# Performance work log

Hardware: AMD Instinct MI355X
Metric: run time of the kernel (lower is better)

Reference implementation:

```python
import jax, jax.numpy as jnp
import numpy as np
from jax import lax

LAMBD = 1.0
KAPPA = 0.1
N_ITERS = 400  # fixed unroll count; PGD converges well within this for these scales


def _project_simplex(v):
    # Euclidean projection of each row of v onto {w : w >= 0, sum(w) = 1}.
    n = v.shape[-1]
    u = -jnp.sort(-v, axis=-1)                       # descending sort
    css = jnp.cumsum(u, axis=-1)
    j = jnp.arange(1, n + 1, dtype=v.dtype)
    cond = u + (1.0 - css) / j > 0                   # monotone condition; rho = #True
    rho = jnp.sum(cond, axis=-1, keepdims=True)      # [B,1], always >= 1
    css_rho = jnp.take_along_axis(css, rho - 1, axis=-1)
    tau = (css_rho - 1.0) / rho.astype(v.dtype)
    return jnp.maximum(v - tau, 0.0)


def _solve_robust_mvo(mu, U, A):
    # min_w -mu'w + kappa*||A w||_2 + (lambd/2)*||U w||_2^2  s.t. w in simplex
    B, n = mu.shape
    G1 = jnp.einsum('bij,bik->bjk', U, U)            # U^T U, [B,n,n]
    G2 = jnp.einsum('bij,bik->bjk', A, A)            # A^T A, [B,n,n]
    # Lipschitz upper bound via Frobenius norms -> safe fixed step size
    froU2 = jnp.sum(U * U, axis=(-2, -1), keepdims=False)[:, None]   # ||U||_F^2, [B,1]
    froA = jnp.sqrt(jnp.sum(A * A, axis=(-2, -1)))[:, None]          # ||A||_F,   [B,1]
    step = 1.0 / (LAMBD * froU2 + KAPPA * froA + 1.0)

    w0 = jnp.full((B, n), 1.0 / n, dtype=mu.dtype)

    def body(w, _):
        g1w = jnp.einsum('bij,bj->bi', G1, w)        # U^T U w
        g2w = jnp.einsum('bij,bj->bi', G2, w)        # A^T A w
        nrm = jnp.sqrt(jnp.maximum(jnp.sum(w * g2w, axis=-1, keepdims=True), 1e-12))
        grad = -mu + LAMBD * g1w + KAPPA * g2w / nrm
        w_new = _project_simplex(w - step * grad)
        return w_new, None

    w, _ = lax.scan(body, w0, None, length=N_ITERS)
    # mirror the torch post-processing: clamp + renormalize
    w = jnp.maximum(w, 0.0)
    return w / (jnp.sum(w, axis=-1, keepdims=True) + 1e-12)


def setup_inputs() -> dict:
    key = jax.random.key(0)
    k1, k2, k3 = jax.random.split(key, 3)
    B, n = 512, 256
    mu = jax.random.normal(k1, (B, n), dtype=jnp.float32)
    U = jax.random.normal(k2, (B, n, n), dtype=jnp.float32)
    A = jax.random.normal(k3, (B, n, n), dtype=jnp.float32)
    return {"mu": mu, "U": U, "A": A}


def reference(mu, U, A):
    return _solve_robust_mvo(mu, U, A)
```

## Files before the change

kernel.cpp:

```cpp
#include <hip/hip_runtime.h>
#include <math.h>

#define NB 512
#define NN 256
#define N_ITERS 400
#define KAPPA_F 0.1f

typedef _Float16 half2_t __attribute__((ext_vector_type(2)));
typedef _Float16 half8_t __attribute__((ext_vector_type(8)));

__device__ inline float fdot2f(half2_t a, half2_t b, float c) {
#if __has_builtin(__builtin_amdgcn_fdot2)
  return __builtin_amdgcn_fdot2(a, b, c, false);
#else
  return (float)a.x * (float)b.x + (float)a.y * (float)b.y + c;
#endif
}


#define PAIR(V, K) __builtin_shufflevector(V, V, 2*(K), 2*(K)+1)

template <int CTRL>
__device__ inline float dpp_addt(float v) {
  int s = __builtin_amdgcn_update_dpp(0, __float_as_int(v), CTRL, 0xF, 0xF, true);
  return v + __int_as_float(s);
}
__device__ inline float wave_sum(float v) {
  v = dpp_addt<0xB1>(v);
  v = dpp_addt<0x4E>(v);
  v = dpp_addt<0x141>(v);
  v = dpp_addt<0x140>(v);
  v += __shfl_xor(v, 16, 64);
  v += __shfl_xor(v, 32, 64);
  return v;
}
__device__ inline void wave_sum2(float& a, float& b) {
  a = dpp_addt<0xB1>(a);  b = dpp_addt<0xB1>(b);
  a = dpp_addt<0x4E>(a);  b = dpp_addt<0x4E>(b);
  a = dpp_addt<0x141>(a); b = dpp_addt<0x141>(b);
  a = dpp_addt<0x140>(a); b = dpp_addt<0x140>(b);
  a += __shfl_xor(a, 16, 64); b += __shfl_xor(b, 16, 64);
  a += __shfl_xor(a, 32, 64); b += __shfl_xor(b, 32, 64);
}

#define DECLROW(P) half2_t P##0,P##1,P##2,P##3,P##4,P##5,P##6,P##7, \
                           P##8,P##9,P##10,P##11,P##12,P##13,P##14,P##15;

#define ZA(J) cA##J.x=0.f; cA##J.y=0.f; cA##J.z=0.f; cA##J.w=0.f;
#define ZB(J) cB##J.x=0.f; cB##J.y=0.f; cB##J.z=0.f; cB##J.w=0.f;
#define ZALL() ZA(0) ZA(1) ZA(2) ZA(3) ZA(4) ZA(5) ZA(6) ZA(7) \
               ZB(0) ZB(1) ZB(2) ZB(3) ZB(4) ZB(5) ZB(6) ZB(7)
#define GMA(J,F) { cA##J.x=fmaf(a0,F.x,cA##J.x); cA##J.y=fmaf(a0,F.y,cA##J.y); \
                   cA##J.z=fmaf(a0,F.z,cA##J.z); cA##J.w=fmaf(a0,F.w,cA##J.w); }
#define GMB(J,F) { cB##J.x=fmaf(a1,F.x,cB##J.x); cB##J.y=fmaf(a1,F.y,cB##J.y); \
                   cB##J.z=fmaf(a1,F.z,cB##J.z); cB##J.w=fmaf(a1,F.w,cB##J.w); }

#define GRAM2(SRC, RB, DOFRO) do { \
  const float4* __restrict__ src4 = (const float4*)(SRC); \
  ZALL() \
  float4 st0 = src4[t], st1 = src4[512 + t]; \
  _Pragma("unroll 1") \
  for (int kt = 0; kt < 16; ++kt) { \
    __syncthreads(); \
    ((float4*)As)[t] = st0; \
    ((float4*)As)[512 + t] = st1; \
    if (DOFRO) { fro += st0.x*st0.x + st0.y*st0.y + st0.z*st0.z + st0.w*st0.w; \
                 fro += st1.x*st1.x + st1.y*st1.y + st1.z*st1.z + st1.w*st1.w; } \
    __syncthreads(); \
    if (kt < 15) { st0 = src4[(kt+1)*1024 + t]; st1 = src4[(kt+1)*1024 + 512 + t]; } \
    _Pragma("unroll 1") \
    for (int k = 0; k < 16; ++k) { \
      const float* rowp = As + k * NN; \
      float a0 = rowp[(RB) + lane]; \
      float a1 = rowp[(RB) + 64 + lane]; \
      const float4* rp4 = (const float4*)(rowp + 32 * wv); \
      { float4 f0=rp4[0], f1=rp4[1], f2=rp4[2], f3=rp4[3]; \
        GMA(0,f0) GMA(1,f1) GMA(2,f2) GMA(3,f3) \
        GMB(0,f0) GMB(1,f1) GMB(2,f2) GMB(3,f3) } \
      { float4 f4=rp4[4], f5=rp4[5], f6=rp4[6], f7=rp4[7]; \
        GMA(4,f4) GMA(5,f5) GMA(6,f6) GMA(7,f7) \
        GMB(4,f4) GMB(5,f5) GMB(6,f6) GMB(7,f7) } \
    } \
  } \
} while (0)

#define GRAM1(SRC, RB, DOFRO) do { \
  const float4* __restrict__ src4 = (const float4*)(SRC); \
  ZA(0) ZA(1) ZA(2) ZA(3) ZA(4) ZA(5) ZA(6) ZA(7) \
  float4 st = src4[t]; \
  _Pragma("unroll 1") \
  for (int kt = 0; kt < 32; ++kt) { \
    __syncthreads(); \
    ((float4*)As)[t] = st; \
    if (DOFRO) fro += st.x*st.x + st.y*st.y + st.z*st.z + st.w*st.w; \
    __syncthreads(); \
    if (kt < 31) st = src4[(kt + 1) * 512 + t]; \
    _Pragma("unroll 1") \
    for (int k = 0; k < 8; ++k) { \
      const float* rowp = As + k * NN; \
      float a0 = rowp[(RB) + lane]; \
      const float4* rp4 = (const float4*)(rowp + 32 * wv); \
      { float4 f0=rp4[0], f1=rp4[1], f2=rp4[2], f3=rp4[3]; \
        GMA(0,f0) GMA(1,f1) GMA(2,f2) GMA(3,f3) } \
      { float4 f4=rp4[4], f5=rp4[5], f6=rp4[6], f7=rp4[7]; \
        GMA(4,f4) GMA(5,f5) GMA(6,f6) GMA(7,f7) } \
    } \
  } \
} while (0)

#define PACK4(PA, PB, C, J4, DIAG) { \
  float x0=C.x, x1=C.y, x2=C.z, x3=C.w; \
  const int cb = 32*wv + 4*(J4); \
  if (cb+0==row_) { DIAG[row_]=x0; x0=0.f; } \
  if (cb+1==row_) { DIAG[row_]=x1; x1=0.f; } \
  if (cb+2==row_) { DIAG[row_]=x2; x2=0.f; } \
  if (cb+3==row_) { DIAG[row_]=x3; x3=0.f; } \
  PA.x=(_Float16)x0; PA.y=(_Float16)x1; \
  PB.x=(_Float16)x2; PB.y=(_Float16)x3; }

#define PACKROW(P, CP, DIAG) { \
  PACK4(P##0,  P##1,  c##CP##0, 0, DIAG) \
  PACK4(P##2,  P##3,  c##CP##1, 1, DIAG) \
  PACK4(P##4,  P##5,  c##CP##2, 2, DIAG) \
  PACK4(P##6,  P##7,  c##CP##3, 3, DIAG) \
  PACK4(P##8,  P##9,  c##CP##4, 4, DIAG) \
  PACK4(P##10, P##11, c##CP##5, 5, DIAG) \
  PACK4(P##12, P##13, c##CP##6, 6, DIAG) \
  PACK4(P##14, P##15, c##CP##7, 7, DIAG) }

#define DOTROW(ACC, P) \
  ACC = fdot2f(P##0,  PAIR(uh0,0), ACC); \
  ACC = fdot2f(P##1,  PAIR(uh0,1), ACC); \
  ACC = fdot2f(P##2,  PAIR(uh0,2), ACC); \
  ACC = fdot2f(P##3,  PAIR(uh0,3), ACC); \
  ACC = fdot2f(P##4,  PAIR(uh1,0), ACC); \
  ACC = fdot2f(P##5,  PAIR(uh1,1), ACC); \
  ACC = fdot2f(P##6,  PAIR(uh1,2), ACC); \
  ACC = fdot2f(P##7,  PAIR(uh1,3), ACC); \
  ACC = fdot2f(P##8,  PAIR(uh2,0), ACC); \
  ACC = fdot2f(P##9,  PAIR(uh2,1), ACC); \
  ACC = fdot2f(P##10, PAIR(uh2,2), ACC); \
  ACC = fdot2f(P##11, PAIR(uh2,3), ACC); \
  ACC = fdot2f(P##12, PAIR(uh3,0), ACC); \
  ACC = fdot2f(P##13, PAIR(uh3,1), ACC); \
  ACC = fdot2f(P##14, PAIR(uh3,2), ACC); \
  ACC = fdot2f(P##15, PAIR(uh3,3), ACC);

#define COMB(I) { \
  const int rr = 64 * (I) + lane; \
  float2 x0 = parts[rr],          x1 = parts[NN + rr]; \
  float2 x2 = parts[2*NN + rr],   x3 = parts[3*NN + rr]; \
  float2 x4 = parts[4*NN + rr],   x5 = parts[5*NN + rr]; \
  float2 x6 = parts[6*NN + rr],   x7 = parts[7*NN + rr]; \
  q1##I = ((x0.x+x1.x)+(x2.x+x3.x))+((x4.x+x5.x)+(x6.x+x7.x)); \
  q2##I = ((x0.y+x1.y)+(x2.y+x3.y))+((x4.y+x5.y)+(x6.y+x7.y)); }

__global__
__attribute__((amdgpu_flat_work_group_size(512, 512)))
__attribute__((amdgpu_waves_per_eu(1, 2)))
void mvo_kernel(const float* __restrict__ mu,
                const float* __restrict__ U,
                const float* __restrict__ A,
                float* __restrict__ out)
{
  __shared__ alignas(16) float2 parts[8 * NN];
  __shared__ alignas(16) float    wsf[NN];
  __shared__ alignas(16) _Float16 whs[NN];
  __shared__ float mus[NN];
  __shared__ float diag1[NN];
  __shared__ float diag2[NN];
  __shared__ float dslot[8];
  __shared__ float slotA[8];
  __shared__ float slotB[8];
  __shared__ float taus;
  __shared__ int   doneflag;

  float* As = (float*)parts;

  const int t    = threadIdx.x;
  const int b    = blockIdx.x;
  const int lane = t & 63;
  const int wv   = t >> 6;

  const float* __restrict__ Ub = U + (size_t)b * NN * NN;
  const float* __restrict__ Ab = A + (size_t)b * NN * NN;

  if (t == 0) { doneflag = 0; taus = -1e30f; }
  if (t < NN) mus[t] = mu[b * NN + t];

  DECLROW(e0_) DECLROW(e1_) DECLROW(e2_) DECLROW(e3_)
  DECLROW(h0_) DECLROW(h1_) DECLROW(h2_) DECLROW(h3_)
  float4 cA0,cA1,cA2,cA3,cA4,cA5,cA6,cA7;
  float4 cB0,cB1,cB2,cB3,cB4,cB5,cB6,cB7;
  float fro, d1, d2;

  fro = 0.f;
  GRAM2(Ab, 0, 1);
  { const int row_ = lane;        PACKROW(h0_, A, diag2) }
  { const int row_ = 64 + lane;   PACKROW(h1_, B, diag2) }
  GRAM2(Ab, 128, 0);
  { const int row_ = 128 + lane;  PACKROW(h2_, A, diag2) }
  { const int row_ = 192 + lane;  PACKROW(h3_, B, diag2) }
  d2 = fro;
  fro = 0.f;
  GRAM1(Ub, 0, 1);
  { const int row_ = lane;        PACKROW(e0_, A, diag1) }
  GRAM1(Ub, 64, 0);
  { const int row_ = 64 + lane;   PACKROW(e1_, A, diag1) }
  GRAM1(Ub, 128, 0);
  { const int row_ = 128 + lane;  PACKROW(e2_, A, diag1) }
  GRAM1(Ub, 192, 0);
  { const int row_ = 192 + lane;  PACKROW(e3_, A, diag1) }
  d1 = fro;

  #pragma unroll
  for (int m = 1; m < 64; m <<= 1) {
    d1 += __shfl_xor(d1, m, 64);
    d2 += __shfl_xor(d2, m, 64);
  }
  if (lane == 0) { slotA[wv] = d1; slotB[wv] = d2; }
  if (t < NN) { wsf[t] = 1.0f / 256.0f; whs[t] = (_Float16)(1.0f / 256.0f); }
  __syncthreads();
  float froU2 = 0.f, froA2 = 0.f;
  #pragma unroll
  for (int k = 0; k < 8; ++k) { froU2 += slotA[k]; froA2 += slotB[k]; }
  const float step = 1.0f / (froU2 + KAPPA_F * sqrtf(froA2) + 1.0f);

  const half8_t* whp = (const half8_t*)whs + 4 * wv;
  const int dsel = lane >> 5;

  #pragma unroll 1
  for (int it = 0; it < N_ITERS; ++it) {
    half8_t uh0 = whp[0], uh1 = whp[1], uh2 = whp[2], uh3 = whp[3];
    float p10=0.f, p11=0.f, p12=0.f, p13=0.f;
    float p20=0.f, p21=0.f, p22=0.f, p23=0.f;
    DOTROW(p10, e0_) DOTROW(p11, e1_) DOTROW(p12, e2_) DOTROW(p13, e3_)
    DOTROW(p20, h0_) DOTROW(p21, h1_) DOTROW(p22, h2_) DOTROW(p23, h3_)

    float w_r0 = wsf[lane],       w_r1 = wsf[64 + lane];
    float w_r2 = wsf[128 + lane], w_r3 = wsf[192 + lane];
    if (wv == dsel)     { p10 = fmaf(diag1[lane],     w_r0, p10);
                          p20 = fmaf(diag2[lane],     w_r0, p20); }
    if (wv == 2 + dsel) { p11 = fmaf(diag1[64+lane],  w_r1, p11);
                          p21 = fmaf(diag2[64+lane],  w_r1, p21); }
    if (wv == 4 + dsel) { p12 = fmaf(diag1[128+lane], w_r2, p12);
                          p22 = fmaf(diag2[128+lane], w_r2, p22); }
    if (wv == 6 + dsel) { p13 = fmaf(diag1[192+lane], w_r3, p13);
                          p23 = fmaf(diag2[192+lane], w_r3, p23); }
    float dpart = fmaf(p20, w_r0, fmaf(p21, w_r1, fmaf(p22, w_r2, p23 * w_r3)));
    dpart = wave_sum(dpart);
    parts[wv * NN + lane]       = make_float2(p10, p20);
    parts[wv * NN + 64 + lane]  = make_float2(p11, p21);
    parts[wv * NN + 128 + lane] = make_float2(p12, p22);
    parts[wv * NN + 192 + lane] = make_float2(p13, p23);
    if (lane == 0) dslot[wv] = dpart;
    __syncthreads();

    if (wv == 0) {
      float q10, q11, q12, q13, q20, q21, q22, q23;
      COMB(0) COMB(1) COMB(2) COMB(3)
      float dot = ((dslot[0]+dslot[1])+(dslot[2]+dslot[3]))
                + ((dslot[4]+dslot[5])+(dslot[6]+dslot[7]));
      float nrm = sqrtf(fmaxf(dot, 1e-12f));
      float kon = KAPPA_F / nrm;
      float v0 = w_r0 - step * (q10 + kon * q20 - mus[lane]);
      float v1 = w_r1 - step * (q11 + kon * q21 - mus[64 + lane]);
      float v2 = w_r2 - step * (q12 + kon * q22 - mus[128 + lane]);
      float v3 = w_r3 - step * (q13 + kon * q23 - mus[192 + lane]);
      float tau = taus;
      float cprev = -1.f;
      #pragma unroll 1
      for (int ms = 0; ms < 24; ++ms) {
        float s2 = (v0 > tau ? v0 : 0.f) + (v1 > tau ? v1 : 0.f)
                 + (v2 > tau ? v2 : 0.f) + (v3 > tau ? v3 : 0.f);
        float c2 = (v0 > tau ? 1.f : 0.f) + (v1 > tau ? 1.f : 0.f)
                 + (v2 > tau ? 1.f : 0.f) + (v3 > tau ? 1.f : 0.f);
        wave_sum2(s2, c2);
        if (c2 == cprev) break;
        tau = (s2 - 1.0f) / c2;
        cprev = c2;
      }
      float nw0 = fmaxf(v0 - tau, 0.f);
      float nw1 = fmaxf(v1 - tau, 0.f);
      float nw2 = fmaxf(v2 - tau, 0.f);
      float nw3 = fmaxf(v3 - tau, 0.f);
      int same = (nw0 == w_r0) && (nw1 == w_r1) && (nw2 == w_r2) && (nw3 == w_r3);
      int conv = __all(same);
      wsf[lane]       = nw0; wsf[64 + lane]  = nw1;
      wsf[128 + lane] = nw2; wsf[192 + lane] = nw3;
      whs[lane]       = (_Float16)nw0; whs[64 + lane]  = (_Float16)nw1;
      whs[128 + lane] = (_Float16)nw2; whs[192 + lane] = (_Float16)nw3;
      if (lane == 0) { taus = tau; doneflag = conv; }
    }
    __syncthreads();
    if (doneflag) break;
  }

  if (wv == 0) {
    float w_0 = wsf[lane],       w_1 = wsf[64 + lane];
    float w_2 = wsf[128 + lane], w_3 = wsf[192 + lane];
    float s = wave_sum(w_0 + w_1 + w_2 + w_3);
    float inv = 1.0f / (s + 1e-12f);
    float* ob = out + b * NN;
    ob[lane]        = w_0 * inv;
    ob[64 + lane]   = w_1 * inv;
    ob[128 + lane]  = w_2 * inv;
    ob[192 + lane]  = w_3 * inv;
  }
}

extern "C" void kernel_launch(void* const* d_in, const int* in_sizes, int n_in,
                              void* d_out, int out_size, void* d_ws, size_t ws_size,
                              hipStream_t stream) {
  const float* mu = (const float*)d_in[0];
  const float* U  = (const float*)d_in[1];
  const float* A  = (const float*)d_in[2];
  float* out = (float*)d_out;
  hipLaunchKernelGGL(mvo_kernel, dim3(NB), dim3(512), 0, stream, mu, U, A, out);
}
```

Measured before the change: 2.133 ms.

## Replicate projection step in every wave to drop second barrier per iteration

Instead of wave 0 alone combining partial sums and projecting onto the simplex while the other waves wait, every wave now does the redundant combine, norm and projection itself. Each wave keeps w in registers and writes its fp16 copy to a private LDS slot. The partial-sum buffer is double-buffered, so only one __syncthreads per iteration remains. The wave reduction now uses row_bcast DPP plus a readlane instead of shuffles, giving a uniform scalar result. This trades eight-fold redundant projection work and extra LDS reads for fewer barriers and less idle time.

```diff
diff --git a/kernel.cpp b/kernel.cpp
--- a/kernel.cpp
+++ b/kernel.cpp
@@ -20,27 +20,19 @@
 
 #define PAIR(V, K) __builtin_shufflevector(V, V, 2*(K), 2*(K)+1)
 
-template <int CTRL>
-__device__ inline float dpp_addt(float v) {
-  int s = __builtin_amdgcn_update_dpp(0, __float_as_int(v), CTRL, 0xF, 0xF, true);
+template <int CTRL, int RMASK>
+__device__ inline float dpp_add(float v) {
+  int s = __builtin_amdgcn_update_dpp(0, __float_as_int(v), CTRL, RMASK, 0xF, true);
   return v + __int_as_float(s);
 }
-__device__ inline float wave_sum(float v) {
-  v = dpp_addt<0xB1>(v);
-  v = dpp_addt<0x4E>(v);
-  v = dpp_addt<0x141>(v);
-  v = dpp_addt<0x140>(v);
-  v += __shfl_xor(v, 16, 64);
-  v += __shfl_xor(v, 32, 64);
-  return v;
-}
-__device__ inline void wave_sum2(float& a, float& b) {
-  a = dpp_addt<0xB1>(a);  b = dpp_addt<0xB1>(b);
-  a = dpp_addt<0x4E>(a);  b = dpp_addt<0x4E>(b);
-  a = dpp_addt<0x141>(a); b = dpp_addt<0x141>(b);
-  a = dpp_addt<0x140>(a); b = dpp_addt<0x140>(b);
-  a += __shfl_xor(a, 16, 64); b += __shfl_xor(b, 16, 64);
-  a += __shfl_xor(a, 32, 64); b += __shfl_xor(b, 32, 64);
+__device__ inline float wave_sum_sgpr(float v) {
+  v = dpp_add<0xB1, 0xF>(v);
+  v = dpp_add<0x4E, 0xF>(v);
+  v = dpp_add<0x141,0xF>(v);
+  v = dpp_add<0x140,0xF>(v);
+  v = dpp_add<0x142,0xA>(v);
+  v = dpp_add<0x143,0xC>(v);
+  return __int_as_float(__builtin_amdgcn_readlane(__float_as_int(v), 63));
 }
 
 #define DECLROW(P) half2_t P##0,P##1,P##2,P##3,P##4,P##5,P##6,P##7, \
@@ -146,12 +138,12 @@
   ACC = fdot2f(P##14, PAIR(uh3,2), ACC); \
   ACC = fdot2f(P##15, PAIR(uh3,3), ACC);
 
-#define COMB(I) { \
+#define COMB(PP, I) { \
   const int rr = 64 * (I) + lane; \
-  float2 x0 = parts[rr],          x1 = parts[NN + rr]; \
-  float2 x2 = parts[2*NN + rr],   x3 = parts[3*NN + rr]; \
-  float2 x4 = parts[4*NN + rr],   x5 = parts[5*NN + rr]; \
-  float2 x6 = parts[6*NN + rr],   x7 = parts[7*NN + rr]; \
+  float2 x0 = PP[rr],          x1 = PP[NN + rr]; \
+  float2 x2 = PP[2*NN + rr],   x3 = PP[3*NN + rr]; \
+  float2 x4 = PP[4*NN + rr],   x5 = PP[5*NN + rr]; \
+  float2 x6 = PP[6*NN + rr],   x7 = PP[7*NN + rr]; \
   q1##I = ((x0.x+x1.x)+(x2.x+x3.x))+((x4.x+x5.x)+(x6.x+x7.x)); \
   q2##I = ((x0.y+x1.y)+(x2.y+x3.y))+((x4.y+x5.y)+(x6.y+x7.y)); }
 
@@ -163,19 +155,15 @@
                 const float* __restrict__ A,
                 float* __restrict__ out)
 {
-  __shared__ alignas(16) float2 parts[8 * NN];
-  __shared__ alignas(16) float    wsf[NN];
-  __shared__ alignas(16) _Float16 whs[NN];
+  __shared__ alignas(16) float2 partsbuf[2][8 * NN];
+  __shared__ alignas(16) _Float16 whsl[8 * NN];
   __shared__ float mus[NN];
   __shared__ float diag1[NN];
   __shared__ float diag2[NN];
-  __shared__ float dslot[8];
   __shared__ float slotA[8];
   __shared__ float slotB[8];
-  __shared__ float taus;
-  __shared__ int   doneflag;
-
-  float* As = (float*)parts;
+
+  float* As = (float*)&partsbuf[0][0];
 
   const int t    = threadIdx.x;
   const int b    = blockIdx.x;
@@ -185,7 +173,6 @@
   const float* __restrict__ Ub = U + (size_t)b * NN * NN;
   const float* __restrict__ Ab = A + (size_t)b * NN * NN;
 
-  if (t == 0) { doneflag = 0; taus = -1e30f; }
   if (t < NN) mus[t] = mu[b * NN + t];
 
   DECLROW(e0_) DECLROW(e1_) DECLROW(e2_) DECLROW(e3_)
@@ -219,93 +206,109 @@
     d2 += __shfl_xor(d2, m, 64);
   }
   if (lane == 0) { slotA[wv] = d1; slotB[wv] = d2; }
-  if (t < NN) { wsf[t] = 1.0f / 256.0f; whs[t] = (_Float16)(1.0f / 256.0f); }
   __syncthreads();
   float froU2 = 0.f, froA2 = 0.f;
   #pragma unroll
   for (int k = 0; k < 8; ++k) { froU2 += slotA[k]; froA2 += slotB[k]; }
   const float step = 1.0f / (froU2 + KAPPA_F * sqrtf(froA2) + 1.0f);
 
-  const half8_t* whp = (const half8_t*)whs + 4 * wv;
   const int dsel = lane >> 5;
+  const float mu_r0 = mus[lane],       mu_r1 = mus[64 + lane];
+  const float mu_r2 = mus[128 + lane], mu_r3 = mus[192 + lane];
+  const float fdU0 = (wv == dsel)     ? diag1[lane]       : 0.f;
+  const float fdA0 = (wv == dsel)     ? diag2[lane]       : 0.f;
+  const float fdU1 = (wv == 2 + dsel) ? diag1[64 + lane]  : 0.f;
+  const float fdA1 = (wv == 2 + dsel) ? diag2[64 + lane]  : 0.f;
+  const float fdU2 = (wv == 4 + dsel) ? diag1[128 + lane] : 0.f;
+  const float fdA2 = (wv == 4 + dsel) ? diag2[128 + lane] : 0.f;
+  const float fdU3 = (wv == 6 + dsel) ? diag1[192 + lane] : 0.f;
+  const float fdA3 = (wv == 6 + dsel) ? diag2[192 + lane] : 0.f;
+
+  float w_r0 = 1.0f/256.0f, w_r1 = 1.0f/256.0f, w_r2 = 1.0f/256.0f, w_r3 = 1.0f/256.0f;
+  half8_t uh0;
+  { const _Float16 hv = (_Float16)(1.0f/256.0f);
+    uh0[0]=hv; uh0[1]=hv; uh0[2]=hv; uh0[3]=hv;
+    uh0[4]=hv; uh0[5]=hv; uh0[6]=hv; uh0[7]=hv; }
+  half8_t uh1 = uh0, uh2 = uh0, uh3 = uh0;
+
+  _Float16* myslot = whsl + (wv << 8);
+  const half8_t* myslot8 = (const half8_t*)myslot;
+  float tau_ws = -1e30f;
+  int pb = 0;
 
   #pragma unroll 1
   for (int it = 0; it < N_ITERS; ++it) {
-    half8_t uh0 = whp[0], uh1 = whp[1], uh2 = whp[2], uh3 = whp[3];
     float p10=0.f, p11=0.f, p12=0.f, p13=0.f;
     float p20=0.f, p21=0.f, p22=0.f, p23=0.f;
     DOTROW(p10, e0_) DOTROW(p11, e1_) DOTROW(p12, e2_) DOTROW(p13, e3_)
     DOTROW(p20, h0_) DOTROW(p21, h1_) DOTROW(p22, h2_) DOTROW(p23, h3_)
-
-    float w_r0 = wsf[lane],       w_r1 = wsf[64 + lane];
-    float w_r2 = wsf[128 + lane], w_r3 = wsf[192 + lane];
-    if (wv == dsel)     { p10 = fmaf(diag1[lane],     w_r0, p10);
-                          p20 = fmaf(diag2[lane],     w_r0, p20); }
-    if (wv == 2 + dsel) { p11 = fmaf(diag1[64+lane],  w_r1, p11);
-                          p21 = fmaf(diag2[64+lane],  w_r1, p21); }
-    if (wv == 4 + dsel) { p12 = fmaf(diag1[128+lane], w_r2, p12);
-                          p22 = fmaf(diag2[128+lane], w_r2, p22); }
-    if (wv == 6 + dsel) { p13 = fmaf(diag1[192+lane], w_r3, p13);
-                          p23 = fmaf(diag2[192+lane], w_r3, p23); }
-    float dpart = fmaf(p20, w_r0, fmaf(p21, w_r1, fmaf(p22, w_r2, p23 * w_r3)));
-    dpart = wave_sum(dpart);
-    parts[wv * NN + lane]       = make_float2(p10, p20);
-    parts[wv * NN + 64 + lane]  = make_float2(p11, p21);
-    parts[wv * NN + 128 + lane] = make_float2(p12, p22);
-    parts[wv * NN + 192 + lane] = make_float2(p13, p23);
-    if (lane == 0) dslot[wv] = dpart;
+    p10 = fmaf(fdU0, w_r0, p10);  p20 = fmaf(fdA0, w_r0, p20);
+    p11 = fmaf(fdU1, w_r1, p11);  p21 = fmaf(fdA1, w_r1, p21);
+    p12 = fmaf(fdU2, w_r2, p12);  p22 = fmaf(fdA2, w_r2, p22);
+    p13 = fmaf(fdU3, w_r3, p13);  p23 = fmaf(fdA3, w_r3, p23);
+
+    float2* P = &partsbuf[pb][0];
+    P[wv * NN + lane]       = make_float2(p10, p20);
+    P[wv * NN + 64 + lane]  = make_float2(p11, p21);
+    P[wv * NN + 128 + lane] = make_float2(p12, p22);
+    P[wv * NN + 192 + lane] = make_float2(p13, p23);
     __syncthreads();
 
-    if (wv == 0) {
-      float q10, q11, q12, q13, q20, q21, q22, q23;
-      COMB(0) COMB(1) COMB(2) COMB(3)
-      float dot = ((dslot[0]+dslot[1])+(dslot[2]+dslot[3]))
-                + ((dslot[4]+dslot[5])+(dslot[6]+dslot[7]));
-      float nrm = sqrtf(fmaxf(dot, 1e-12f));
-      float kon = KAPPA_F / nrm;
-      float v0 = w_r0 - step * (q10 + kon * q20 - mus[lane]);
-      float v1 = w_r1 - step * (q11 + kon * q21 - mus[64 + lane]);
-      float v2 = w_r2 - step * (q12 + kon * q22 - mus[128 + lane]);
-      float v3 = w_r3 - step * (q13 + kon * q23 - mus[192 + lane]);
-      float tau = taus;
-      float cprev = -1.f;
-      #pragma unroll 1
-      for (int ms = 0; ms < 24; ++ms) {
-        float s2 = (v0 > tau ? v0 : 0.f) + (v1 > tau ? v1 : 0.f)
-                 + (v2 > tau ? v2 : 0.f) + (v3 > tau ? v3 : 0.f);
-        float c2 = (v0 > tau ? 1.f : 0.f) + (v1 > tau ? 1.f : 0.f)
-                 + (v2 > tau ? 1.f : 0.f) + (v3 > tau ? 1.f : 0.f);
-        wave_sum2(s2, c2);
-        if (c2 == cprev) break;
-        tau = (s2 - 1.0f) / c2;
-        cprev = c2;
-      }
-      float nw0 = fmaxf(v0 - tau, 0.f);
-      float nw1 = fmaxf(v1 - tau, 0.f);
-      float nw2 = fmaxf(v2 - tau, 0.f);
-      float nw3 = fmaxf(v3 - tau, 0.f);
-      int same = (nw0 == w_r0) && (nw1 == w_r1) && (nw2 == w_r2) && (nw3 == w_r3);
-      int conv = __all(same);
-      wsf[lane]       = nw0; wsf[64 + lane]  = nw1;
-      wsf[128 + lane] = nw2; wsf[192 + lane] = nw3;
-      whs[lane]       = (_Float16)nw0; whs[64 + lane]  = (_Float16)nw1;
-      whs[128 + lane] = (_Float16)nw2; whs[192 + lane] = (_Float16)nw3;
-      if (lane == 0) { taus = tau; doneflag = conv; }
+    float q10, q11, q12, q13, q20, q21, q22, q23;
+    COMB(P, 0) COMB(P, 1) COMB(P, 2) COMB(P, 3)
+    float dot = wave_sum_sgpr(
+        fmaf(q20, w_r0, fmaf(q21, w_r1, fmaf(q22, w_r2, q23 * w_r3))));
+    float nrm = sqrtf(fmaxf(dot, 1e-12f));
+    float kon = KAPPA_F / nrm;
+    float v0 = w_r0 - step * (q10 + kon * q20 - mu_r0);
+    float v1 = w_r1 - step * (q11 + kon * q21 - mu_r1);
+    float v2 = w_r2 - step * (q12 + kon * q22 - mu_r2);
+    float v3 = w_r3 - step * (q13 + kon * q23 - mu_r3);
+
+    float tau = tau_ws;
+    float cprev = -1.f;
+    #pragma unroll 1
+    for (int ms = 0; ms < 24; ++ms) {
+      float s2 = (v0 > tau ? v0 : 0.f) + (v1 > tau ? v1 : 0.f)
+               + (v2 > tau ? v2 : 0.f) + (v3 > tau ? v3 : 0.f);
+      float c2 = (v0 > tau ? 1.f : 0.f) + (v1 > tau ? 1.f : 0.f)
+               + (v2 > tau ? 1.f : 0.f) + (v3 > tau ? 1.f : 0.f);
+      s2 = wave_sum_sgpr(s2);
+      c2 = wave_sum_sgpr(c2);
+      if (c2 == cprev) break;
+      tau = (s2 - 1.0f) / c2;
+      cprev = c2;
     }
-    __syncthreads();
-    if (doneflag) break;
+    float nw0 = fmaxf(v0 - tau, 0.f);
+    float nw1 = fmaxf(v1 - tau, 0.f);
+    float nw2 = fmaxf(v2 - tau, 0.f);
+    float nw3 = fmaxf(v3 - tau, 0.f);
+    int conv = __all((nw0 == w_r0) && (nw1 == w_r1) &&
+                     (nw2 == w_r2) && (nw3 == w_r3));
+    w_r0 = nw0; w_r1 = nw1; w_r2 = nw2; w_r3 = nw3;
+    tau_ws = tau;
+
+    myslot[lane]        = (_Float16)nw0;
+    myslot[64 + lane]   = (_Float16)nw1;
+    myslot[128 + lane]  = (_Float16)nw2;
+    myslot[192 + lane]  = (_Float16)nw3;
+    uh0 = myslot8[4 * wv + 0];
+    uh1 = myslot8[4 * wv + 1];
+    uh2 = myslot8[4 * wv + 2];
+    uh3 = myslot8[4 * wv + 3];
+
+    pb ^= 1;
+    if (conv) break;
   }
 
   if (wv == 0) {
-    float w_0 = wsf[lane],       w_1 = wsf[64 + lane];
-    float w_2 = wsf[128 + lane], w_3 = wsf[192 + lane];
-    float s = wave_sum(w_0 + w_1 + w_2 + w_3);
+    float s = wave_sum_sgpr(w_r0 + w_r1 + w_r2 + w_r3);
     float inv = 1.0f / (s + 1e-12f);
     float* ob = out + b * NN;
-    ob[lane]        = w_0 * inv;
-    ob[64 + lane]   = w_1 * inv;
-    ob[128 + lane]  = w_2 * inv;
-    ob[192 + lane]  = w_3 * inv;
+    ob[lane]        = w_r0 * inv;
+    ob[64 + lane]   = w_r1 * inv;
+    ob[128 + lane]  = w_r2 * inv;
+    ob[192 + lane]  = w_r3 * inv;
   }
 }
 
```

After: 2.828 ms. 32.6% more time.
